# Kernel tuning notes

Hardware: AMD Instinct MI355X
Metric: run time of the kernel (lower is better)

## Reference

```python
import jax, jax.numpy as jnp
import numpy as np

H = 16            # num_attention_heads
START_RATIO = 0.1
RECENT_RATIO = 0.4
THETA = 10000.0
CHUNK = 256       # hard-coded chunk_size in source
CLIP = 1e4        # nan_to_num posinf/neginf bound


def _rope_cos_sin(T, D, dtype):
    inv_freq = 1.0 / (THETA ** (jnp.arange(0, D, 2, dtype=jnp.float32) / D))
    freqs = jnp.arange(T, dtype=jnp.float32)[:, None] * inv_freq[None, :]  # [T, D/2]
    emb = jnp.concatenate([freqs, freqs], axis=-1)                          # [T, D]
    return jnp.cos(emb).astype(dtype), jnp.sin(emb).astype(dtype)


def _apply_rope(x, cos, sin):
    # x: [B,H,T,D]; cos/sin: [T,D] broadcast over B,H
    d = x.shape[-1] // 2
    rot = jnp.concatenate([-x[..., d:], x[..., :d]], axis=-1)
    return x * cos + rot * sin


def setup_inputs() -> dict:
    key = jax.random.key(0)
    k0, k1, k2, k3, k4 = jax.random.split(key, 5)
    B, T, Dm = 1, 2048, 2048
    scale = 1.0 / np.sqrt(Dm).astype(np.float32)
    return {
        "hidden_states": jax.random.normal(k0, (B, T, Dm), jnp.float32),
        "Wq": jax.random.normal(k1, (Dm, Dm), jnp.float32) * scale,
        "Wk": jax.random.normal(k2, (Dm, Dm), jnp.float32) * scale,
        "Wv": jax.random.normal(k3, (Dm, Dm), jnp.float32) * scale,
        "Wo": jax.random.normal(k4, (Dm, Dm), jnp.float32) * scale,
    }


def reference(hidden_states, Wq, Wk, Wv, Wo):
    B, T, Dm = hidden_states.shape
    D = Dm // H
    hs = jnp.nan_to_num(hidden_states, nan=0.0, posinf=CLIP, neginf=-CLIP)

    def proj(W):  # torch Linear: x @ W.T, then [B,T,H,D] -> [B,H,T,D]
        return (hs @ W.T).reshape(B, T, H, D).transpose(0, 2, 1, 3)

    q, k, v = proj(Wq), proj(Wk), proj(Wv)
    cos, sin = _rope_cos_sin(T, D, hs.dtype)
    q = _apply_rope(q, cos, sin)
    k = _apply_rope(k, cos, sin)

    # start+recent keep mask (past_key_value=None -> k_len == T)
    k_len = T
    sb = max(0, min(int(START_RATIO * k_len), k_len))
    rb = max(0, min(int(RECENT_RATIO * k_len), k_len - sb))
    pos = jnp.arange(k_len)
    keep = (pos < sb) | (pos >= k_len - rb)          # [K]

    MIN = jnp.finfo(hs.dtype).min
    scores = jnp.einsum('bhqd,bhkd->bhqk', q, k) / jnp.sqrt(jnp.asarray(D, hs.dtype))
    scores = jnp.where(keep, scores, MIN)
    probs = jax.nn.softmax(scores, axis=-1)          # [B,H,T,K]

    # CaM merge of evicted V into recent window, driven by the LAST query row.
    evict = k_len - rb                               # static python int
    last = probs[..., -1, :]                         # [B,H,K]
    mean_attn = last[..., evict + 1:].mean(axis=-1) + 1e-6
    p = jnp.clip(last[..., evict] / mean_attn, 0.0, 1.0)
    p = jnp.nan_to_num(p, nan=0.0, posinf=1.0, neginf=0.0)
    u = jax.random.uniform(jax.random.key(42), p.shape, p.dtype)
    bern = (u < p).astype(v.dtype)                   # [B,H]
    v_e = v[..., evict, :] * bern[..., None] / rb    # [B,H,D]
    v_merged = v.at[..., evict + 1:, :].add(v_e[..., None, :])

    # Chunked loop effect: only the last chunk's AV uses merged V.
    last_start = ((T - 1) // CHUNK) * CHUNK
    out_pre = jnp.einsum('bhqk,bhkd->bhqd', probs[:, :, :last_start], v)
    out_last = jnp.einsum('bhqk,bhkd->bhqd', probs[:, :, last_start:], v_merged)
    out = jnp.concatenate([out_pre, out_last], axis=2)   # [B,H,T,D]

    out = out.transpose(0, 2, 1, 3).reshape(B, T, Dm) @ Wo.T
    return jnp.nan_to_num(out, nan=0.0, posinf=CLIP, neginf=-CLIP)
```

## Files before the change

kernel.cpp:

```cpp
#include <hip/hip_runtime.h>
#include <stdint.h>

#define T_SEQ 2048
#define DM    2048
#define NH    16
#define HD    128
#define SB    204
#define EV    1229
#define RB    819
#define NRECF 818.0f
#define LAST_START 1792
#define SCALE 0.08838834764831845f

typedef __attribute__((ext_vector_type(8))) short short8;
typedef __attribute__((ext_vector_type(4))) short short4v;
typedef __attribute__((ext_vector_type(4))) float f32x4;

__device__ __forceinline__ unsigned short f2bf(float f) {
  uint32_t u = __float_as_uint(f);
  u += 0x7fffu + ((u >> 16) & 1u);
  return (unsigned short)(u >> 16);
}
__device__ __forceinline__ float bf2f(unsigned short s) {
  return __uint_as_float(((uint32_t)s) << 16);
}
__device__ __forceinline__ void gload16(const void* g, void* l) {
  __builtin_amdgcn_global_load_lds((const __attribute__((address_space(1))) void*)g,
                                   (__attribute__((address_space(3))) void*)l,
                                   16, 0, 0);
}
__device__ __forceinline__ float n2n(float v) {
  if (isnan(v)) return 0.0f;
  if (isinf(v)) return v > 0.0f ? 10000.0f : -10000.0f;
  return v;
}

__global__ __launch_bounds__(256) void cvt_kernel(
    const float* __restrict__ hs, const float* __restrict__ wq,
    const float* __restrict__ wk, const float* __restrict__ wv,
    const float* __restrict__ wo, unsigned short* __restrict__ hsb,
    unsigned short* __restrict__ wqb, unsigned short* __restrict__ wkb,
    unsigned short* __restrict__ wvb, unsigned short* __restrict__ wob,
    float* __restrict__ cst, float* __restrict__ snt) {
  if (blockIdx.x >= 20480) {
    int idx = (blockIdx.x - 20480) * 256 + threadIdx.x;
    int t = idx >> 6, i = idx & 63;
    float inv = exp2f(-(float)i * 0.20761871929904988f);
    float ang = (float)t * inv;
    float s, c;
    sincosf(ang, &s, &c);
    cst[idx] = c;
    snt[idx] = s;
    return;
  }
  int gid = blockIdx.x * 256 + threadIdx.x;
  int region = gid >> 20;
  int off4 = (gid & 1048575) * 4;
  const float* src; unsigned short* dst;
  switch (region) {
    case 0: src = hs; dst = hsb; break;
    case 1: src = wq; dst = wqb; break;
    case 2: src = wk; dst = wkb; break;
    case 3: src = wv; dst = wvb; break;
    default: src = wo; dst = wob; break;
  }
  float4 v = *(const float4*)(src + off4);
  if (region == 0) { v.x = n2n(v.x); v.y = n2n(v.y); v.z = n2n(v.z); v.w = n2n(v.w); }
  ushort4 o;
  o.x = f2bf(v.x); o.y = f2bf(v.y); o.z = f2bf(v.z); o.w = f2bf(v.w);
  *(ushort4*)(dst + off4) = o;
}

__device__ __forceinline__ void gemm_mainloop64(
    const unsigned short* __restrict__ A, const unsigned short* __restrict__ B,
    unsigned short* As, unsigned short* Bs, int m0, int n0, int k0, int ksteps,
    int tid, f32x4 (&acc)[4][4]) {
  int w = tid >> 6, lane = tid & 63;
  int wm = w >> 1, wn = w & 1;
  int q4 = lane >> 4, r = lane & 15;
  f32x4 zero = {0.f, 0.f, 0.f, 0.f};
  #pragma unroll
  for (int mi = 0; mi < 4; mi++)
    #pragma unroll
    for (int ni = 0; ni < 4; ni++) acc[mi][ni] = zero;
  int srow = w * 32 + (lane >> 3);
  int swz = ((lane & 7) ^ (lane >> 3)) * 16;
  const char* Ag = (const char*)(A + (size_t)(m0 + srow) * DM) + swz + k0 * 2;
  const char* Bg = (const char*)(B + (size_t)(n0 + srow) * DM) + swz + k0 * 2;
  unsigned short* Asl = As + w * 2048;
  unsigned short* Bsl = Bs + w * 2048;
  for (int s = 0; s < ksteps; s++) {
    __syncthreads();
    #pragma unroll
    for (int g = 0; g < 4; g++) {
      gload16(Ag + g * (8 * DM * 2), Asl + g * 512);
      gload16(Bg + g * (8 * DM * 2), Bsl + g * 512);
    }
    Ag += 128; Bg += 128;
    __syncthreads();
    #pragma unroll
    for (int kh = 0; kh < 2; kh++) {
      int pcs = ((kh * 4 + q4) ^ (r & 7)) * 8;
      short8 a[4], b[4];
      #pragma unroll
      for (int mi = 0; mi < 4; mi++)
        a[mi] = *(const short8*)(As + (wm * 64 + mi * 16 + r) * 64 + pcs);
      #pragma unroll
      for (int ni = 0; ni < 4; ni++)
        b[ni] = *(const short8*)(Bs + ((ni & 1) * 64 + wn * 32 + (ni >> 1) * 16 + r) * 64 + pcs);
      #pragma unroll
      for (int mi = 0; mi < 4; mi++)
        #pragma unroll
        for (int ni = 0; ni < 4; ni++)
          acc[mi][ni] = __builtin_amdgcn_mfma_f32_16x16x32_bf16(a[mi], b[ni], acc[mi][ni], 0, 0, 0);
    }
  }
}

__global__ __launch_bounds__(256, 3) void gemm_qkv_kernel(
    const unsigned short* __restrict__ hsb, const unsigned short* __restrict__ wqb,
    const unsigned short* __restrict__ wkb, const unsigned short* __restrict__ wvb,
    const float* __restrict__ cst, const float* __restrict__ snt,
    unsigned short* __restrict__ qbf, unsigned short* __restrict__ kbf,
    unsigned short* __restrict__ vbT) {
  __shared__ __align__(16) unsigned short LDSBUF[17408];
  unsigned short* As = LDSBUF;
  unsigned short* Bs = LDSBUF + 8192;
  int y = blockIdx.y;
  int z, mi;
  if (y < 16)      { z = 0; mi = y; }
  else if (y < 25) { z = 1; mi = y - 16; }
  else             { z = 2; mi = y - 25; }
  if (z) mi = (mi < 2) ? mi : mi + 7;
  const unsigned short* B = (z == 0) ? wqb : (z == 1) ? wkb : wvb;
  int m0 = mi * 128, n0 = blockIdx.x * 128;
  f32x4 acc[4][4];
  gemm_mainloop64(hsb, B, As, Bs, m0, n0, 0, DM / 64, threadIdx.x, acc);
  int tid = threadIdx.x, w = tid >> 6, lane = tid & 63;
  int wm = w >> 1, wn = w & 1, q4 = lane >> 4, r = lane & 15;
  int h = n0 >> 7;
  if (z < 2) {
    unsigned short* dst = (z == 0) ? qbf : kbf;
    #pragma unroll
    for (int mj = 0; mj < 4; mj++)
      #pragma unroll
      for (int p = 0; p < 2; p++) {
        int d = wn * 32 + p * 16 + r;
        #pragma unroll
        for (int g = 0; g < 4; g++) {
          int t = m0 + wm * 64 + mj * 16 + q4 * 4 + g;
          float c = cst[t * 64 + d], s = snt[t * 64 + d];
          float x0 = acc[mj][2 * p][g], x1 = acc[mj][2 * p + 1][g];
          dst[((size_t)h * T_SEQ + t) * HD + d]      = f2bf(x0 * c - x1 * s);
          dst[((size_t)h * T_SEQ + t) * HD + d + 64] = f2bf(x1 * c + x0 * s);
        }
      }
  } else {
    __syncthreads();
    #pragma unroll
    for (int mj = 0; mj < 4; mj++)
      #pragma unroll
      for (int ni = 0; ni < 4; ni++) {
        int c = (ni & 1) * 64 + wn * 32 + (ni >> 1) * 16 + r;
        int tl = wm * 64 + mj * 16 + q4 * 4;
        short4v pv;
        pv[0] = (short)f2bf(acc[mj][ni][0]);
        pv[1] = (short)f2bf(acc[mj][ni][1]);
        pv[2] = (short)f2bf(acc[mj][ni][2]);
        pv[3] = (short)f2bf(acc[mj][ni][3]);
        *(short4v*)(LDSBUF + c * 136 + tl) = pv;
      }
    __syncthreads();
    int d = tid >> 1, th = tid & 1;
    unsigned short* gdst = vbT + ((size_t)h * HD + d) * T_SEQ + m0 + th * 64;
    const unsigned short* lsrc = LDSBUF + d * 136 + th * 64;
    #pragma unroll
    for (int j = 0; j < 8; j++)
      *(short8*)(gdst + j * 8) = *(const short8*)(lsrc + j * 8);
  }
}

__device__ __forceinline__ void attn_body2(
    int kb, const unsigned short* Kt0, const unsigned short* Kt1,
    const unsigned short* Vt0, const unsigned short* Vt1,
    const unsigned short* ind0, const unsigned short* ind1,
    unsigned short* Ps0, unsigned short* Ps1,
    const short8 (&aq)[4], f32x4 (&o)[8], f32x4& o9, float (&evf)[4],
    int q4, int r) {
  f32x4 zero = {0.f, 0.f, 0.f, 0.f};
  int rsw = (r >> 1) & 3;
  f32x4 sA0 = zero, sA1 = zero, sB0 = zero, sB1 = zero;
  __builtin_amdgcn_s_setprio(1);
  #pragma unroll
  for (int c = 0; c < 4; c++) {
    int pc = ((c * 4 + q4) ^ r) * 8;
    short8 kA0 = *(const short8*)(Kt0 + r * 128 + pc);
    short8 kA1 = *(const short8*)(Kt0 + (16 + r) * 128 + pc);
    short8 kB0 = *(const short8*)(Kt1 + r * 128 + pc);
    short8 kB1 = *(const short8*)(Kt1 + (16 + r) * 128 + pc);
    sA0 = __builtin_amdgcn_mfma_f32_16x16x32_bf16(aq[c], kA0, sA0, 0, 0, 0);
    sA1 = __builtin_amdgcn_mfma_f32_16x16x32_bf16(aq[c], kA1, sA1, 0, 0, 0);
    sB0 = __builtin_amdgcn_mfma_f32_16x16x32_bf16(aq[c], kB0, sB0, 0, 0, 0);
    sB1 = __builtin_amdgcn_mfma_f32_16x16x32_bf16(aq[c], kB1, sB1, 0, 0, 0);
  }
  __builtin_amdgcn_s_setprio(0);
  int kgA0 = kb + r, kgA1 = kb + 16 + r, kgB0 = kb + 32 + r, kgB1 = kb + 48 + r;
  bool keepA0 = (kgA0 < SB) || (kgA0 >= EV);
  bool keepA1 = (kgA1 < SB) || (kgA1 >= EV);
  bool keepB0 = (kgB0 < SB) || (kgB0 >= EV);
  bool keepB1 = (kgB1 < SB) || (kgB1 >= EV);
  #pragma unroll
  for (int g = 0; g < 4; g++) {
    float pA0 = keepA0 ? __expf(fmaf(sA0[g], SCALE, -8.0f)) : 0.0f;
    float pA1 = keepA1 ? __expf(fmaf(sA1[g], SCALE, -8.0f)) : 0.0f;
    float pB0 = keepB0 ? __expf(fmaf(sB0[g], SCALE, -8.0f)) : 0.0f;
    float pB1 = keepB1 ? __expf(fmaf(sB1[g], SCALE, -8.0f)) : 0.0f;
    if (kb == 1216 && kgA0 == EV) evf[g] = pA0;
    int row = q4 * 4 + g;
    int psw = (row >> 1) & 3;
    int c0 = (((r >> 3) ^ psw) * 8) + (r & 7);
    int c1 = ((((r >> 3) + 2) ^ psw) * 8) + (r & 7);
    Ps0[row * 32 + c0] = f2bf(pA0);
    Ps0[row * 32 + c1] = f2bf(pA1);
    Ps1[row * 32 + c0] = f2bf(pB0);
    Ps1[row * 32 + c1] = f2bf(pB1);
  }
  short8 pa0 = *(const short8*)(Ps0 + r * 32 + (q4 ^ rsw) * 8);
  short8 pa1 = *(const short8*)(Ps1 + r * 32 + (q4 ^ rsw) * 8);
  __builtin_amdgcn_s_setprio(1);
  #pragma unroll
  for (int ni = 0; ni < 8; ni++) {
    short8 bv0 = *(const short8*)(Vt0 + (ni * 16 + r) * 32 + (q4 ^ rsw) * 8);
    short8 bv1 = *(const short8*)(Vt1 + (ni * 16 + r) * 32 + (q4 ^ rsw) * 8);
    o[ni] = __builtin_amdgcn_mfma_f32_16x16x32_bf16(pa0, bv0, o[ni], 0, 0, 0);
    o[ni] = __builtin_amdgcn_mfma_f32_16x16x32_bf16(pa1, bv1, o[ni], 0, 0, 0);
  }
  short8 bi0 = *(const short8*)(ind0 + r * 32 + (q4 ^ rsw) * 8);
  short8 bi1 = *(const short8*)(ind1 + r * 32 + (q4 ^ rsw) * 8);
  o9 = __builtin_amdgcn_mfma_f32_16x16x32_bf16(pa0, bi0, o9, 0, 0, 0);
  o9 = __builtin_amdgcn_mfma_f32_16x16x32_bf16(pa1, bi1, o9, 0, 0, 0);
  __builtin_amdgcn_s_setprio(0);
}

__global__ __launch_bounds__(512, 1) void attn_kernel(
    const unsigned short* __restrict__ qbf, const unsigned short* __restrict__ kbf,
    const unsigned short* __restrict__ vbT, unsigned short* __restrict__ atb,
    float* __restrict__ attnf_s, float* __restrict__ Ssum, float* __restrict__ lst) {
  __shared__ __align__(16) unsigned short KtS[2][2][4096];
  __shared__ __align__(16) unsigned short VtS[2][2][4096];
  __shared__ __align__(16) unsigned short Ps[8][2][512];
  __shared__ __align__(16) unsigned short Ind[3 * 512];
  int tid = threadIdx.x, w8 = tid >> 6, lane = tid & 63;
  int q4 = lane >> 4, r = lane & 15;
  int bid = blockIdx.x;
  int xcd = bid & 7, j = bid >> 3;
  int h = xcd * 2 + (j >> 4);
  int qx = j & 15;
  int qb = qx * 128 + w8 * 16;

  for (int idx = tid; idx < 3 * 512; idx += 512) {
    int v = idx >> 9, n = (idx >> 5) & 15, jj = idx & 31;
    float val = 0.f;
    if (n == 0) val = 1.f;
    else if (n == 1) val = (v == 1) ? (jj >= 14 ? 1.f : 0.f) : (v == 2 ? 1.f : 0.f);
    Ind[v * 512 + n * 32 + (((jj >> 3) ^ ((n >> 1) & 3)) * 8) + (jj & 7)] = f2bf(val);
  }

  short8 aq[4];
  {
    const unsigned short* qrow = qbf + ((size_t)h * T_SEQ + qb + r) * HD;
    #pragma unroll
    for (int c = 0; c < 4; c++) aq[c] = *(const short8*)(qrow + c * 32 + q4 * 8);
  }
  f32x4 zero = {0.f, 0.f, 0.f, 0.f};
  f32x4 o[8], o9;
  #pragma unroll
  for (int ni = 0; ni < 8; ni++) o[ni] = zero;
  o9 = zero;
  float evf[4] = {0.f, 0.f, 0.f, 0.f};

  const char* Kbase = (const char*)(kbf + (size_t)h * T_SEQ * HD);
  int krow = w8 * 4 + q4;
  const char* Kg = Kbase + krow * 256 + ((r ^ (krow & 15)) * 16);
  const char* Vbase = (const char*)(vbT + (size_t)h * HD * T_SEQ);
  int vsrc = ((lane & 3) ^ ((lane >> 3) & 3)) * 16;
  const char* Vg = Vbase + (size_t)(w8 * 16 + (lane >> 2)) * 4096 + vsrc;

  auto issue_chunk = [&](int ci, int db) {
    int kb = (ci < 4) ? ci * 64 : 1216 + (ci - 4) * 64;
    gload16(Kg + kb * 256,        &KtS[db][0][w8 * 512]);
    gload16(Kg + (kb + 32) * 256, &KtS[db][1][w8 * 512]);
    gload16(Vg + kb * 2,          &VtS[db][0][w8 * 512]);
    gload16(Vg + (kb + 32) * 2,   &VtS[db][1][w8 * 512]);
  };

  issue_chunk(0, 0);
  for (int ci = 0; ci < 17; ci++) {
    int db = ci & 1;
    int kb = (ci < 4) ? ci * 64 : 1216 + (ci - 4) * 64;
    const unsigned short* indA = Ind + ((ci < 4) ? 0 : (ci == 4) ? 512 : 1024);
    const unsigned short* indB = Ind + ((ci < 4) ? 0 : 1024);
    __syncthreads();
    if (ci < 16) issue_chunk(ci + 1, db ^ 1);
    attn_body2(kb, KtS[db][0], KtS[db][1], VtS[db][0], VtS[db][1],
               indA, indB, &Ps[w8][0][0], &Ps[w8][1][0], aq, o, o9, evf, q4, r);
  }

  float invl[4], srn[4], evn[4];
  #pragma unroll
  for (int g = 0; g < 4; g++) {
    float l  = __shfl(o9[g], lane & 48, 64);
    float sr = __shfl(o9[g], (lane & 48) | 1, 64);
    float ev = __shfl(evf[g], (lane & 48) | 13, 64);
    invl[g] = 1.0f / l;
    srn[g] = sr * invl[g];
    evn[g] = ev * invl[g];
  }
  if (qx < 14) {
    #pragma unroll
    for (int ni = 0; ni < 8; ni++)
      #pragma unroll
      for (int g = 0; g < 4; g++)
        atb[(size_t)(qb + q4 * 4 + g) * DM + h * HD + ni * 16 + r] = f2bf(o[ni][g] * invl[g]);
  } else {
    #pragma unroll
    for (int ni = 0; ni < 8; ni++)
      #pragma unroll
      for (int g = 0; g < 4; g++)
        attnf_s[(size_t)(qb - LAST_START + q4 * 4 + g) * DM + h * HD + ni * 16 + r] = o[ni][g] * invl[g];
  }
  if (r == 0) {
    #pragma unroll
    for (int g = 0; g < 4; g++) {
      int t = qb + q4 * 4 + g;
      if (t >= LAST_START) Ssum[h * 256 + (t - LAST_START)] = srn[g];
      if (t == T_SEQ - 1) { lst[h * 2] = evn[g]; lst[h * 2 + 1] = srn[g]; }
    }
  }
}

__device__ __forceinline__ void tf_round(uint32_t& x0, uint32_t& x1, int rot) {
  x0 += x1;
  x1 = (x1 << rot) | (x1 >> (32 - rot));
  x1 ^= x0;
}
__device__ __forceinline__ float bern_scale(int hh, const float* lst) {
  const uint32_t k0 = 0u, k1 = 42u, k2 = 0x1BD11BDAu ^ k0 ^ k1;
  uint32_t x0 = (uint32_t)(hh & 7), x1 = (uint32_t)((hh & 7) + 8);
  x0 += k0; x1 += k1;
  tf_round(x0, x1, 13); tf_round(x0, x1, 15); tf_round(x0, x1, 26); tf_round(x0, x1, 6);
  x0 += k1; x1 += k2 + 1u;
  tf_round(x0, x1, 17); tf_round(x0, x1, 29); tf_round(x0, x1, 16); tf_round(x0, x1, 24);
  x0 += k2; x1 += k0 + 2u;
  tf_round(x0, x1, 13); tf_round(x0, x1, 15); tf_round(x0, x1, 26); tf_round(x0, x1, 6);
  x0 += k0; x1 += k1 + 3u;
  tf_round(x0, x1, 17); tf_round(x0, x1, 29); tf_round(x0, x1, 16); tf_round(x0, x1, 24);
  x0 += k1; x1 += k2 + 4u;
  tf_round(x0, x1, 13); tf_round(x0, x1, 15); tf_round(x0, x1, 26); tf_round(x0, x1, 6);
  x0 += k2; x1 += k0 + 5u;
  uint32_t bits = (hh < 8) ? x0 : x1;
  float u = __uint_as_float((bits >> 9) | 0x3f800000u) - 1.0f;
  float evp = lst[hh * 2], srp = lst[hh * 2 + 1];
  float mean = srp * (1.0f / NRECF) + 1e-6f;
  float p = evp / mean;
  p = fminf(fmaxf(p, 0.0f), 1.0f);
  if (!(p == p)) p = 0.0f;
  return (u < p) ? (1.0f / (float)RB) : 0.0f;
}

__global__ __launch_bounds__(256) void fixup_kernel(
    const float* __restrict__ attnf_s, const float* __restrict__ Ssum,
    const float* __restrict__ lst, const unsigned short* __restrict__ vbT,
    unsigned short* __restrict__ atb) {
  int idx = (blockIdx.x * 256 + threadIdx.x) * 4;
  int t2 = idx >> 11, n = idx & 2047;
  int h = n >> 7, d = n & 127;
  float bsc = bern_scale(h, lst) * Ssum[h * 256 + t2];
  float4 v = *(const float4*)(attnf_s + idx);
  const unsigned short* vrow = vbT + ((size_t)h * HD + d) * T_SEQ + EV;
  ushort4 ov;
  ov.x = f2bf(v.x + bsc * bf2f(vrow[0]));
  ov.y = f2bf(v.y + bsc * bf2f(vrow[T_SEQ]));
  ov.z = f2bf(v.z + bsc * bf2f(vrow[2 * T_SEQ]));
  ov.w = f2bf(v.w + bsc * bf2f(vrow[3 * T_SEQ]));
  *(ushort4*)(atb + (size_t)(t2 + LAST_START) * DM + n) = ov;
}

__global__ __launch_bounds__(512, 2) void gemm_out_kernel(
    const unsigned short* __restrict__ atb, const unsigned short* __restrict__ wob,
    float* __restrict__ out) {
  __shared__ __align__(16) unsigned short LDSBUF[32768];
  int tid = threadIdx.x;
  int grp = tid >> 8;
  int ltid = tid & 255;
  unsigned short* As = LDSBUF + grp * 16384;
  unsigned short* Bs = As + 8192;
  int m0 = blockIdx.y * 128, n0 = blockIdx.x * 128;
  f32x4 acc[4][4];
  gemm_mainloop64(atb, wob, As, Bs, m0, n0, grp * 1024, 16, ltid, acc);
  float* Cx = (float*)LDSBUF;
  __syncthreads();
  if (grp) {
    #pragma unroll
    for (int mi = 0; mi < 4; mi++)
      #pragma unroll
      for (int ni = 0; ni < 4; ni++)
        #pragma unroll
        for (int g = 0; g < 4; g++)
          Cx[(mi * 16 + ni * 4 + g) * 256 + ltid] = acc[mi][ni][g];
  }
  __syncthreads();
  if (!grp) {
    int w = ltid >> 6, lane = ltid & 63;
    int wm = w >> 1, wn = w & 1, q4 = lane >> 4, r = lane & 15;
    #pragma unroll
    for (int mi = 0; mi < 4; mi++)
      #pragma unroll
      for (int ni = 0; ni < 4; ni++) {
        int c = n0 + (ni & 1) * 64 + wn * 32 + (ni >> 1) * 16 + r;
        #pragma unroll
        for (int g = 0; g < 4; g++) {
          int t = m0 + wm * 64 + mi * 16 + q4 * 4 + g;
          out[(size_t)t * DM + c] = n2n(acc[mi][ni][g] + Cx[(mi * 16 + ni * 4 + g) * 256 + ltid]);
        }
      }
  }
}

extern "C" void kernel_launch(void* const* d_in, const int* in_sizes, int n_in,
                              void* d_out, int out_size, void* d_ws, size_t ws_size,
                              hipStream_t stream) {
  const float* hs = (const float*)d_in[0];
  const float* Wq = (const float*)d_in[1];
  const float* Wk = (const float*)d_in[2];
  const float* Wv = (const float*)d_in[3];
  const float* Wo = (const float*)d_in[4];
  char* ws = (char*)d_ws;
  const size_t MB = 1024 * 1024;
  unsigned short* hsb = (unsigned short*)(ws + 0);
  unsigned short* wqb = (unsigned short*)(ws + 8 * MB);
  unsigned short* wkb = (unsigned short*)(ws + 16 * MB);
  unsigned short* wvb = (unsigned short*)(ws + 24 * MB);
  unsigned short* wob = (unsigned short*)(ws + 32 * MB);
  unsigned short* qbf = (unsigned short*)(ws + 40 * MB);
  unsigned short* kbf = (unsigned short*)(ws + 48 * MB);
  unsigned short* vbT = (unsigned short*)(ws + 56 * MB);
  unsigned short* atb = (unsigned short*)(ws + 64 * MB);
  float* attnf_s = (float*)(ws + 72 * MB);
  float* cst = (float*)(ws + 106 * MB);
  float* snt = (float*)(ws + 106 * MB + 524288);
  float* Ssum = (float*)(ws + 107 * MB);
  float* lst = (float*)(ws + 107 * MB + 16384);

  cvt_kernel<<<20992, 256, 0, stream>>>(hs, Wq, Wk, Wv, Wo, hsb, wqb, wkb, wvb, wob, cst, snt);
  gemm_qkv_kernel<<<dim3(16, 34), 256, 0, stream>>>(hsb, wqb, wkb, wvb, cst, snt, qbf, kbf, vbT);
  attn_kernel<<<256, 512, 0, stream>>>(qbf, kbf, vbT, atb, attnf_s, Ssum, lst);
  fixup_kernel<<<512, 256, 0, stream>>>(attnf_s, Ssum, lst, vbT, atb);
  gemm_out_kernel<<<dim3(16, 16), 512, 0, stream>>>(atb, wob, (float*)d_out);
}
```

Before: 233.4 us.

## Replace split-K output GEMM with 64x128 tiles and no LDS reduction

The output projection GEMM drops its intra-block split-K scheme, where two 256-thread groups each covered half of K and were summed through LDS. It now uses 256-thread blocks with 64x128 tiles over the full K range, launched on a 16x32 grid. This removes the LDS reduction and extra barriers, doubles the block count for better CU coverage, and lowers LDS use so more blocks fit per CU. The cost is a longer serial K loop per block and less operand reuse per tile.

```diff
diff --git a/kernel.cpp b/kernel.cpp
--- a/kernel.cpp
+++ b/kernel.cpp
@@ -112,6 +112,52 @@
       for (int mi = 0; mi < 4; mi++)
         #pragma unroll
         for (int ni = 0; ni < 4; ni++)
+          acc[mi][ni] = __builtin_amdgcn_mfma_f32_16x16x32_bf16(a[mi], b[ni], acc[mi][ni], 0, 0, 0);
+    }
+  }
+}
+
+__device__ __forceinline__ void gemm_mainloop_m64(
+    const unsigned short* __restrict__ A, const unsigned short* __restrict__ B,
+    unsigned short* As, unsigned short* Bs, int m0, int n0, int k0, int ksteps,
+    int tid, f32x4 (&acc)[4][2]) {
+  int w = tid >> 6, lane = tid & 63;
+  int q4 = lane >> 4, r = lane & 15;
+  f32x4 zero = {0.f, 0.f, 0.f, 0.f};
+  #pragma unroll
+  for (int mi = 0; mi < 4; mi++)
+    #pragma unroll
+    for (int ni = 0; ni < 2; ni++) acc[mi][ni] = zero;
+  int srowA = w * 16 + (lane >> 3);
+  int srowB = w * 32 + (lane >> 3);
+  int swz = ((lane & 7) ^ (lane >> 3)) * 16;
+  const char* Ag = (const char*)(A + (size_t)(m0 + srowA) * DM) + swz + k0 * 2;
+  const char* Bg = (const char*)(B + (size_t)(n0 + srowB) * DM) + swz + k0 * 2;
+  unsigned short* Asl = As + w * 1024;
+  unsigned short* Bsl = Bs + w * 2048;
+  for (int s = 0; s < ksteps; s++) {
+    __syncthreads();
+    gload16(Ag, Asl);
+    gload16(Ag + (8 * DM * 2), Asl + 512);
+    #pragma unroll
+    for (int g = 0; g < 4; g++)
+      gload16(Bg + g * (8 * DM * 2), Bsl + g * 512);
+    Ag += 128; Bg += 128;
+    __syncthreads();
+    #pragma unroll
+    for (int kh = 0; kh < 2; kh++) {
+      int pcs = ((kh * 4 + q4) ^ (r & 7)) * 8;
+      short8 a[4], b[2];
+      #pragma unroll
+      for (int mi = 0; mi < 4; mi++)
+        a[mi] = *(const short8*)(As + (mi * 16 + r) * 64 + pcs);
+      #pragma unroll
+      for (int ni = 0; ni < 2; ni++)
+        b[ni] = *(const short8*)(Bs + (ni * 64 + w * 16 + r) * 64 + pcs);
+      #pragma unroll
+      for (int mi = 0; mi < 4; mi++)
+        #pragma unroll
+        for (int ni = 0; ni < 2; ni++)
           acc[mi][ni] = __builtin_amdgcn_mfma_f32_16x16x32_bf16(a[mi], b[ni], acc[mi][ni], 0, 0, 0);
     }
   }
@@ -386,45 +432,28 @@
   *(ushort4*)(atb + (size_t)(t2 + LAST_START) * DM + n) = ov;
 }
 
-__global__ __launch_bounds__(512, 2) void gemm_out_kernel(
+__global__ __launch_bounds__(256, 6) void gemm_out_kernel(
     const unsigned short* __restrict__ atb, const unsigned short* __restrict__ wob,
     float* __restrict__ out) {
-  __shared__ __align__(16) unsigned short LDSBUF[32768];
-  int tid = threadIdx.x;
-  int grp = tid >> 8;
-  int ltid = tid & 255;
-  unsigned short* As = LDSBUF + grp * 16384;
-  unsigned short* Bs = As + 8192;
-  int m0 = blockIdx.y * 128, n0 = blockIdx.x * 128;
-  f32x4 acc[4][4];
-  gemm_mainloop64(atb, wob, As, Bs, m0, n0, grp * 1024, 16, ltid, acc);
-  float* Cx = (float*)LDSBUF;
-  __syncthreads();
-  if (grp) {
-    #pragma unroll
-    for (int mi = 0; mi < 4; mi++)
-      #pragma unroll
-      for (int ni = 0; ni < 4; ni++)
-        #pragma unroll
-        for (int g = 0; g < 4; g++)
-          Cx[(mi * 16 + ni * 4 + g) * 256 + ltid] = acc[mi][ni][g];
-  }
-  __syncthreads();
-  if (!grp) {
-    int w = ltid >> 6, lane = ltid & 63;
-    int wm = w >> 1, wn = w & 1, q4 = lane >> 4, r = lane & 15;
-    #pragma unroll
-    for (int mi = 0; mi < 4; mi++)
-      #pragma unroll
-      for (int ni = 0; ni < 4; ni++) {
-        int c = n0 + (ni & 1) * 64 + wn * 32 + (ni >> 1) * 16 + r;
-        #pragma unroll
-        for (int g = 0; g < 4; g++) {
-          int t = m0 + wm * 64 + mi * 16 + q4 * 4 + g;
-          out[(size_t)t * DM + c] = n2n(acc[mi][ni][g] + Cx[(mi * 16 + ni * 4 + g) * 256 + ltid]);
-        }
+  __shared__ __align__(16) unsigned short LDSBUF[12288];
+  unsigned short* As = LDSBUF;
+  unsigned short* Bs = LDSBUF + 4096;
+  int m0 = blockIdx.y * 64, n0 = blockIdx.x * 128;
+  f32x4 acc[4][2];
+  gemm_mainloop_m64(atb, wob, As, Bs, m0, n0, 0, DM / 64, threadIdx.x, acc);
+  int tid = threadIdx.x, w = tid >> 6, lane = tid & 63;
+  int q4 = lane >> 4, r = lane & 15;
+  #pragma unroll
+  for (int mi = 0; mi < 4; mi++)
+    #pragma unroll
+    for (int ni = 0; ni < 2; ni++) {
+      int c = n0 + ni * 64 + w * 16 + r;
+      #pragma unroll
+      for (int g = 0; g < 4; g++) {
+        int t = m0 + mi * 16 + q4 * 4 + g;
+        out[(size_t)t * DM + c] = n2n(acc[mi][ni][g]);
       }
-  }
+    }
 }
 
 extern "C" void kernel_launch(void* const* d_in, const int* in_sizes, int n_in,
@@ -456,5 +485,5 @@
   gemm_qkv_kernel<<<dim3(16, 34), 256, 0, stream>>>(hsb, wqb, wkb, wvb, cst, snt, qbf, kbf, vbT);
   attn_kernel<<<256, 512, 0, stream>>>(qbf, kbf, vbT, atb, attnf_s, Ssum, lst);
   fixup_kernel<<<512, 256, 0, stream>>>(attnf_s, Ssum, lst, vbT, atb);
-  gemm_out_kernel<<<dim3(16, 16), 512, 0, stream>>>(atb, wob, (float*)d_out);
-}
+  gemm_out_kernel<<<dim3(16, 32), 256, 0, stream>>>(atb, wob, (float*)d_out);
+}
```

Result: no change. 236.3 us (+1.2%).

## Split attention key range across two blocks and combine partials in a reduction kernel

Applied to the files above, without the earlier changes.

The attention kernel now splits the kept key chunks between two blocks per query tile, doubling the grid to 512 blocks. Each writes unnormalized fp32 output partials plus row sums, and a new combine kernel adds the two halves, normalizes, applies the CaM merge correction, and writes bf16. The per-chunk body is also split into two 32-key halves sharing one P buffer to cut register pressure, with launch bounds raised to allow more occupancy. The cost is an extra 32 MB of fp32 partial traffic and a larger combine kernel that runs over every row instead of only the last chunk.

```diff
diff --git a/kernel.cpp b/kernel.cpp
--- a/kernel.cpp
+++ b/kernel.cpp
@@ -180,82 +180,65 @@
   }
 }
 
-__device__ __forceinline__ void attn_body2(
-    int kb, const unsigned short* Kt0, const unsigned short* Kt1,
-    const unsigned short* Vt0, const unsigned short* Vt1,
-    const unsigned short* ind0, const unsigned short* ind1,
-    unsigned short* Ps0, unsigned short* Ps1,
+__device__ __forceinline__ void attn_body(
+    int kb, const unsigned short* Kt, const unsigned short* Vt,
+    const unsigned short* indv, unsigned short* Psw,
     const short8 (&aq)[4], f32x4 (&o)[8], f32x4& o9, float (&evf)[4],
     int q4, int r) {
   f32x4 zero = {0.f, 0.f, 0.f, 0.f};
   int rsw = (r >> 1) & 3;
-  f32x4 sA0 = zero, sA1 = zero, sB0 = zero, sB1 = zero;
+  f32x4 s0 = zero, s1 = zero;
   __builtin_amdgcn_s_setprio(1);
   #pragma unroll
   for (int c = 0; c < 4; c++) {
     int pc = ((c * 4 + q4) ^ r) * 8;
-    short8 kA0 = *(const short8*)(Kt0 + r * 128 + pc);
-    short8 kA1 = *(const short8*)(Kt0 + (16 + r) * 128 + pc);
-    short8 kB0 = *(const short8*)(Kt1 + r * 128 + pc);
-    short8 kB1 = *(const short8*)(Kt1 + (16 + r) * 128 + pc);
-    sA0 = __builtin_amdgcn_mfma_f32_16x16x32_bf16(aq[c], kA0, sA0, 0, 0, 0);
-    sA1 = __builtin_amdgcn_mfma_f32_16x16x32_bf16(aq[c], kA1, sA1, 0, 0, 0);
-    sB0 = __builtin_amdgcn_mfma_f32_16x16x32_bf16(aq[c], kB0, sB0, 0, 0, 0);
-    sB1 = __builtin_amdgcn_mfma_f32_16x16x32_bf16(aq[c], kB1, sB1, 0, 0, 0);
+    short8 bk0 = *(const short8*)(Kt + r * 128 + pc);
+    short8 bk1 = *(const short8*)(Kt + (16 + r) * 128 + pc);
+    s0 = __builtin_amdgcn_mfma_f32_16x16x32_bf16(aq[c], bk0, s0, 0, 0, 0);
+    s1 = __builtin_amdgcn_mfma_f32_16x16x32_bf16(aq[c], bk1, s1, 0, 0, 0);
   }
   __builtin_amdgcn_s_setprio(0);
-  int kgA0 = kb + r, kgA1 = kb + 16 + r, kgB0 = kb + 32 + r, kgB1 = kb + 48 + r;
-  bool keepA0 = (kgA0 < SB) || (kgA0 >= EV);
-  bool keepA1 = (kgA1 < SB) || (kgA1 >= EV);
-  bool keepB0 = (kgB0 < SB) || (kgB0 >= EV);
-  bool keepB1 = (kgB1 < SB) || (kgB1 >= EV);
+  int kg0 = kb + r, kg1 = kb + 16 + r;
+  bool keep0 = (kg0 < SB) || (kg0 >= EV);
+  bool keep1 = (kg1 < SB) || (kg1 >= EV);
   #pragma unroll
   for (int g = 0; g < 4; g++) {
-    float pA0 = keepA0 ? __expf(fmaf(sA0[g], SCALE, -8.0f)) : 0.0f;
-    float pA1 = keepA1 ? __expf(fmaf(sA1[g], SCALE, -8.0f)) : 0.0f;
-    float pB0 = keepB0 ? __expf(fmaf(sB0[g], SCALE, -8.0f)) : 0.0f;
-    float pB1 = keepB1 ? __expf(fmaf(sB1[g], SCALE, -8.0f)) : 0.0f;
-    if (kb == 1216 && kgA0 == EV) evf[g] = pA0;
+    float p0 = keep0 ? __expf(fmaf(s0[g], SCALE, -8.0f)) : 0.0f;
+    float p1 = keep1 ? __expf(fmaf(s1[g], SCALE, -8.0f)) : 0.0f;
+    if (kb == 1216 && kg0 == EV) evf[g] = p0;
     int row = q4 * 4 + g;
     int psw = (row >> 1) & 3;
-    int c0 = (((r >> 3) ^ psw) * 8) + (r & 7);
-    int c1 = ((((r >> 3) + 2) ^ psw) * 8) + (r & 7);
-    Ps0[row * 32 + c0] = f2bf(pA0);
-    Ps0[row * 32 + c1] = f2bf(pA1);
-    Ps1[row * 32 + c0] = f2bf(pB0);
-    Ps1[row * 32 + c1] = f2bf(pB1);
-  }
-  short8 pa0 = *(const short8*)(Ps0 + r * 32 + (q4 ^ rsw) * 8);
-  short8 pa1 = *(const short8*)(Ps1 + r * 32 + (q4 ^ rsw) * 8);
+    Psw[row * 32 + (((r >> 3) ^ psw) * 8) + (r & 7)]       = f2bf(p0);
+    Psw[row * 32 + ((((r >> 3) + 2) ^ psw) * 8) + (r & 7)] = f2bf(p1);
+  }
+  short8 pa = *(const short8*)(Psw + r * 32 + (q4 ^ rsw) * 8);
   __builtin_amdgcn_s_setprio(1);
   #pragma unroll
   for (int ni = 0; ni < 8; ni++) {
-    short8 bv0 = *(const short8*)(Vt0 + (ni * 16 + r) * 32 + (q4 ^ rsw) * 8);
-    short8 bv1 = *(const short8*)(Vt1 + (ni * 16 + r) * 32 + (q4 ^ rsw) * 8);
-    o[ni] = __builtin_amdgcn_mfma_f32_16x16x32_bf16(pa0, bv0, o[ni], 0, 0, 0);
-    o[ni] = __builtin_amdgcn_mfma_f32_16x16x32_bf16(pa1, bv1, o[ni], 0, 0, 0);
-  }
-  short8 bi0 = *(const short8*)(ind0 + r * 32 + (q4 ^ rsw) * 8);
-  short8 bi1 = *(const short8*)(ind1 + r * 32 + (q4 ^ rsw) * 8);
-  o9 = __builtin_amdgcn_mfma_f32_16x16x32_bf16(pa0, bi0, o9, 0, 0, 0);
-  o9 = __builtin_amdgcn_mfma_f32_16x16x32_bf16(pa1, bi1, o9, 0, 0, 0);
+    short8 bv = *(const short8*)(Vt + (ni * 16 + r) * 32 + (q4 ^ rsw) * 8);
+    o[ni] = __builtin_amdgcn_mfma_f32_16x16x32_bf16(pa, bv, o[ni], 0, 0, 0);
+  }
+  short8 bind = *(const short8*)(indv + r * 32 + (q4 ^ rsw) * 8);
+  o9 = __builtin_amdgcn_mfma_f32_16x16x32_bf16(pa, bind, o9, 0, 0, 0);
   __builtin_amdgcn_s_setprio(0);
 }
 
-__global__ __launch_bounds__(512, 1) void attn_kernel(
+__global__ __launch_bounds__(512, 4) void attn_kernel(
     const unsigned short* __restrict__ qbf, const unsigned short* __restrict__ kbf,
-    const unsigned short* __restrict__ vbT, unsigned short* __restrict__ atb,
-    float* __restrict__ attnf_s, float* __restrict__ Ssum, float* __restrict__ lst) {
+    const unsigned short* __restrict__ vbT, float* __restrict__ opart,
+    float* __restrict__ lw, float* __restrict__ srw, float* __restrict__ evp) {
   __shared__ __align__(16) unsigned short KtS[2][2][4096];
   __shared__ __align__(16) unsigned short VtS[2][2][4096];
-  __shared__ __align__(16) unsigned short Ps[8][2][512];
+  __shared__ __align__(16) unsigned short Ps[8][512];
   __shared__ __align__(16) unsigned short Ind[3 * 512];
   int tid = threadIdx.x, w8 = tid >> 6, lane = tid & 63;
   int q4 = lane >> 4, r = lane & 15;
   int bid = blockIdx.x;
   int xcd = bid & 7, j = bid >> 3;
-  int h = xcd * 2 + (j >> 4);
-  int qx = j & 15;
+  int h = xcd * 2 + (j >> 5);
+  int rem = j & 31;
+  int qx = rem >> 1;
+  int kz = rem & 1;
   int qb = qx * 128 + w8 * 16;
 
   for (int idx = tid; idx < 3 * 512; idx += 512) {
@@ -294,47 +277,35 @@
     gload16(Vg + (kb + 32) * 2,   &VtS[db][1][w8 * 512]);
   };
 
-  issue_chunk(0, 0);
-  for (int ci = 0; ci < 17; ci++) {
-    int db = ci & 1;
+  int ci0 = kz ? 8 : 0, ci1 = kz ? 17 : 8;
+  issue_chunk(ci0, 0);
+  for (int ci = ci0; ci < ci1; ci++) {
+    int db = (ci - ci0) & 1;
     int kb = (ci < 4) ? ci * 64 : 1216 + (ci - 4) * 64;
     const unsigned short* indA = Ind + ((ci < 4) ? 0 : (ci == 4) ? 512 : 1024);
     const unsigned short* indB = Ind + ((ci < 4) ? 0 : 1024);
     __syncthreads();
-    if (ci < 16) issue_chunk(ci + 1, db ^ 1);
-    attn_body2(kb, KtS[db][0], KtS[db][1], VtS[db][0], VtS[db][1],
-               indA, indB, &Ps[w8][0][0], &Ps[w8][1][0], aq, o, o9, evf, q4, r);
-  }
-
-  float invl[4], srn[4], evn[4];
+    if (ci + 1 < ci1) issue_chunk(ci + 1, db ^ 1);
+    attn_body(kb,      KtS[db][0], VtS[db][0], indA, &Ps[w8][0], aq, o, o9, evf, q4, r);
+    attn_body(kb + 32, KtS[db][1], VtS[db][1], indB, &Ps[w8][0], aq, o, o9, evf, q4, r);
+  }
+
+  float* od = opart + ((size_t)kz << 22);
+  #pragma unroll
+  for (int ni = 0; ni < 8; ni++)
+    #pragma unroll
+    for (int g = 0; g < 4; g++)
+      od[(size_t)(qb + q4 * 4 + g) * DM + h * HD + ni * 16 + r] = o[ni][g];
   #pragma unroll
   for (int g = 0; g < 4; g++) {
     float l  = __shfl(o9[g], lane & 48, 64);
     float sr = __shfl(o9[g], (lane & 48) | 1, 64);
     float ev = __shfl(evf[g], (lane & 48) | 13, 64);
-    invl[g] = 1.0f / l;
-    srn[g] = sr * invl[g];
-    evn[g] = ev * invl[g];
-  }
-  if (qx < 14) {
-    #pragma unroll
-    for (int ni = 0; ni < 8; ni++)
-      #pragma unroll
-      for (int g = 0; g < 4; g++)
-        atb[(size_t)(qb + q4 * 4 + g) * DM + h * HD + ni * 16 + r] = f2bf(o[ni][g] * invl[g]);
-  } else {
-    #pragma unroll
-    for (int ni = 0; ni < 8; ni++)
-      #pragma unroll
-      for (int g = 0; g < 4; g++)
-        attnf_s[(size_t)(qb - LAST_START + q4 * 4 + g) * DM + h * HD + ni * 16 + r] = o[ni][g] * invl[g];
-  }
-  if (r == 0) {
-    #pragma unroll
-    for (int g = 0; g < 4; g++) {
+    if (r == 0) {
       int t = qb + q4 * 4 + g;
-      if (t >= LAST_START) Ssum[h * 256 + (t - LAST_START)] = srn[g];
-      if (t == T_SEQ - 1) { lst[h * 2] = evn[g]; lst[h * 2 + 1] = srn[g]; }
+      lw[(kz * 16 + h) * 2048 + t]  = l;
+      srw[(kz * 16 + h) * 2048 + t] = sr;
+      if (kz == 0 && t == T_SEQ - 1) evp[h] = ev;
     }
   }
 }
@@ -344,7 +315,7 @@
   x1 = (x1 << rot) | (x1 >> (32 - rot));
   x1 ^= x0;
 }
-__device__ __forceinline__ float bern_scale(int hh, const float* lst) {
+__device__ __forceinline__ float bern_scale(int hh, float evn, float srn) {
   const uint32_t k0 = 0u, k1 = 42u, k2 = 0x1BD11BDAu ^ k0 ^ k1;
   uint32_t x0 = (uint32_t)(hh & 7), x1 = (uint32_t)((hh & 7) + 8);
   x0 += k0; x1 += k1;
@@ -360,30 +331,45 @@
   x0 += k2; x1 += k0 + 5u;
   uint32_t bits = (hh < 8) ? x0 : x1;
   float u = __uint_as_float((bits >> 9) | 0x3f800000u) - 1.0f;
-  float evp = lst[hh * 2], srp = lst[hh * 2 + 1];
-  float mean = srp * (1.0f / NRECF) + 1e-6f;
-  float p = evp / mean;
+  float mean = srn * (1.0f / NRECF) + 1e-6f;
+  float p = evn / mean;
   p = fminf(fmaxf(p, 0.0f), 1.0f);
   if (!(p == p)) p = 0.0f;
   return (u < p) ? (1.0f / (float)RB) : 0.0f;
 }
 
-__global__ __launch_bounds__(256) void fixup_kernel(
-    const float* __restrict__ attnf_s, const float* __restrict__ Ssum,
-    const float* __restrict__ lst, const unsigned short* __restrict__ vbT,
-    unsigned short* __restrict__ atb) {
+__global__ __launch_bounds__(256) void combine_kernel(
+    const float* __restrict__ opart, const float* __restrict__ lw,
+    const float* __restrict__ srw, const float* __restrict__ evp,
+    const unsigned short* __restrict__ vbT, unsigned short* __restrict__ atb) {
   int idx = (blockIdx.x * 256 + threadIdx.x) * 4;
-  int t2 = idx >> 11, n = idx & 2047;
+  int t = idx >> 11, n = idx & 2047;
   int h = n >> 7, d = n & 127;
-  float bsc = bern_scale(h, lst) * Ssum[h * 256 + t2];
-  float4 v = *(const float4*)(attnf_s + idx);
-  const unsigned short* vrow = vbT + ((size_t)h * HD + d) * T_SEQ + EV;
+  float l = lw[h * 2048 + t] + lw[(16 + h) * 2048 + t];
+  float invl = 1.0f / l;
+  float4 a = *(const float4*)(opart + idx);
+  float4 b = *(const float4*)(opart + (1 << 22) + idx);
+  float vx = (a.x + b.x) * invl;
+  float vy = (a.y + b.y) * invl;
+  float vz = (a.z + b.z) * invl;
+  float vw = (a.w + b.w) * invl;
+  if (t >= LAST_START) {
+    float l27  = lw[h * 2048 + 2047] + lw[(16 + h) * 2048 + 2047];
+    float sr27 = srw[h * 2048 + 2047] + srw[(16 + h) * 2048 + 2047];
+    float evn = evp[h] / l27;
+    float srn27 = sr27 / l27;
+    float bsc = bern_scale(h, evn, srn27);
+    float srt = (srw[h * 2048 + t] + srw[(16 + h) * 2048 + t]) * invl;
+    float f = srt * bsc;
+    const unsigned short* vrow = vbT + ((size_t)h * HD + d) * T_SEQ + EV;
+    vx += f * bf2f(vrow[0]);
+    vy += f * bf2f(vrow[T_SEQ]);
+    vz += f * bf2f(vrow[2 * T_SEQ]);
+    vw += f * bf2f(vrow[3 * T_SEQ]);
+  }
   ushort4 ov;
-  ov.x = f2bf(v.x + bsc * bf2f(vrow[0]));
-  ov.y = f2bf(v.y + bsc * bf2f(vrow[T_SEQ]));
-  ov.z = f2bf(v.z + bsc * bf2f(vrow[2 * T_SEQ]));
-  ov.w = f2bf(v.w + bsc * bf2f(vrow[3 * T_SEQ]));
-  *(ushort4*)(atb + (size_t)(t2 + LAST_START) * DM + n) = ov;
+  ov.x = f2bf(vx); ov.y = f2bf(vy); ov.z = f2bf(vz); ov.w = f2bf(vw);
+  *(ushort4*)(atb + (size_t)t * DM + n) = ov;
 }
 
 __global__ __launch_bounds__(512, 2) void gemm_out_kernel(
@@ -446,15 +432,17 @@
   unsigned short* kbf = (unsigned short*)(ws + 48 * MB);
   unsigned short* vbT = (unsigned short*)(ws + 56 * MB);
   unsigned short* atb = (unsigned short*)(ws + 64 * MB);
-  float* attnf_s = (float*)(ws + 72 * MB);
+  float* opart = (float*)(ws + 72 * MB);
+  float* lsr = (float*)(ws + 104 * MB);
+  float* lw  = lsr;
+  float* srw = lsr + 65536;
+  float* evp = lsr + 131072;
   float* cst = (float*)(ws + 106 * MB);
   float* snt = (float*)(ws + 106 * MB + 524288);
-  float* Ssum = (float*)(ws + 107 * MB);
-  float* lst = (float*)(ws + 107 * MB + 16384);
 
   cvt_kernel<<<20992, 256, 0, stream>>>(hs, Wq, Wk, Wv, Wo, hsb, wqb, wkb, wvb, wob, cst, snt);
   gemm_qkv_kernel<<<dim3(16, 34), 256, 0, stream>>>(hsb, wqb, wkb, wvb, cst, snt, qbf, kbf, vbT);
-  attn_kernel<<<256, 512, 0, stream>>>(qbf, kbf, vbT, atb, attnf_s, Ssum, lst);
-  fixup_kernel<<<512, 256, 0, stream>>>(attnf_s, Ssum, lst, vbT, atb);
+  attn_kernel<<<512, 512, 0, stream>>>(qbf, kbf, vbT, opart, lw, srw, evp);
+  combine_kernel<<<4096, 256, 0, stream>>>(opart, lw, srw, evp, vbT, atb);
   gemm_out_kernel<<<dim3(16, 16), 512, 0, stream>>>(atb, wob, (float*)d_out);
 }
```

Measured after the change: 239.5 us. 1.03x slower.
